# Optimization experiments

Measured on AMD Instinct MI355X. Metric: run time of the kernel, lower is better.

The kernel has to match this reference:

```python
import jax, jax.numpy as jnp
import numpy as np

N = 400000
NUM_OBJECTS = 80000
LOSS_WEIGHT = 1.0
EPS_W = 1e-5
EPS_A = 1e-7

X_SIGN = jnp.array([1, 1, -1, -1, 1, 1, -1, -1], dtype=jnp.float32)
Y_SIGN = jnp.array([1, -1, -1, 1, 1, -1, -1, 1], dtype=jnp.float32)
Z_SIGN = jnp.array([1, 1, 1, 1, -1, -1, -1, -1], dtype=jnp.float32)


def setup_inputs() -> dict:
    key = jax.random.key(0)
    k1, k2, k3, k4, k5, k6 = jax.random.split(key, 6)
    # 3D boxes: centers spread in front of the camera, positive sizes, yaw in [-pi, pi]
    xyz = jnp.concatenate([
        jax.random.uniform(k1, (N, 2), minval=-20.0, maxval=20.0),  # x, y lateral
        jax.random.uniform(k2, (N, 1), minval=-1.5, maxval=1.5),    # z
    ], axis=1)
    lwh = jax.random.uniform(k3, (N, 3), minval=1.0, maxval=5.0)
    yaw = jax.random.uniform(k4, (N, 1), minval=-np.pi, maxval=np.pi)
    pred_3d_bboxes = jnp.concatenate([xyz, lwh, yaw], axis=1)  # (N, 7)
    # GT 2D boxes [x1, y1, x2, y2] inside a 1600x900 image
    x1y1 = jax.random.uniform(k5, (N, 2)) * jnp.array([1200.0, 600.0])
    wh2d = jax.random.uniform(jax.random.fold_in(k5, 1), (N, 2), minval=20.0, maxval=300.0)
    gt_2d_bboxes = jnp.concatenate([x1y1, x1y1 + wh2d], axis=1)
    # Projection matrices: pinhole intrinsics * axis swap (lidar x-forward -> cam z), + tiny noise
    fx, fy, cx, cy = 1000.0, 1000.0, 800.0, 450.0
    K = jnp.array([[fx, 0.0, cx, 0.0], [0.0, fy, cy, 0.0], [0.0, 0.0, 1.0, 0.0], [0.0, 0.0, 0.0, 1.0]], dtype=jnp.float32)
    swap = jnp.array([[0.0, -1.0, 0.0, 0.0], [0.0, 0.0, -1.0, 0.0], [1.0, 0.0, 0.0, 60.0], [0.0, 0.0, 0.0, 1.0]], dtype=jnp.float32)
    base = K @ swap  # (4, 4)
    lidar2img = base[None] + 0.01 * jax.random.normal(k6, (N, 4, 4), dtype=jnp.float32)
    img_shapes = jnp.ones((N, 2), dtype=jnp.float32) * jnp.array([900.0, 1600.0], dtype=jnp.float32)
    object_ids = jax.random.randint(jax.random.fold_in(key, 7), (N,), 0, NUM_OBJECTS, dtype=jnp.int32)
    return {
        "pred_3d_bboxes": pred_3d_bboxes,
        "gt_2d_bboxes": gt_2d_bboxes,
        "lidar2img": lidar2img,
        "img_shapes": img_shapes,
        "object_ids": object_ids,
    }


def _corners_from_bboxes_3d(b):
    # b: (N, 7) -> (N, 8, 3)
    x, y, z = b[:, 0], b[:, 1], b[:, 2]
    l, w, h = b[:, 3], b[:, 4], b[:, 5]
    yaw = b[:, 6]
    xc = (l[:, None] / 2) * X_SIGN  # (N, 8)
    yc = (w[:, None] / 2) * Y_SIGN
    zc = (h[:, None] / 2) * Z_SIGN
    corners = jnp.stack([xc, yc, zc], axis=1)  # (N, 3, 8)
    c, s = jnp.cos(yaw), jnp.sin(yaw)
    zero, one = jnp.zeros_like(c), jnp.ones_like(c)
    R = jnp.stack([c, -s, zero, s, c, zero, zero, zero, one], axis=1).reshape(-1, 3, 3)
    corners = jnp.einsum('nij,njk->nik', R, corners)  # (N, 3, 8)
    center = jnp.stack([x, y, z], axis=1)[:, :, None]
    return (corners + center).transpose(0, 2, 1)  # (N, 8, 3)


def _giou(pred, gt):
    x1 = jnp.maximum(pred[:, 0], gt[:, 0])
    y1 = jnp.maximum(pred[:, 1], gt[:, 1])
    x2 = jnp.minimum(pred[:, 2], gt[:, 2])
    y2 = jnp.minimum(pred[:, 3], gt[:, 3])
    inter = jnp.maximum(x2 - x1, 0.0) * jnp.maximum(y2 - y1, 0.0)
    pa = (pred[:, 2] - pred[:, 0]) * (pred[:, 3] - pred[:, 1])
    ga = (gt[:, 2] - gt[:, 0]) * (gt[:, 3] - gt[:, 1])
    union = pa + ga - inter + EPS_A
    iou = inter / union
    cx1 = jnp.minimum(pred[:, 0], gt[:, 0])
    cy1 = jnp.minimum(pred[:, 1], gt[:, 1])
    cx2 = jnp.maximum(pred[:, 2], gt[:, 2])
    cy2 = jnp.maximum(pred[:, 3], gt[:, 3])
    c_area = jnp.maximum(cx2 - cx1, 0.0) * jnp.maximum(cy2 - cy1, 0.0) + EPS_A
    return iou - (c_area - union) / c_area


def _loss(pred_3d_bboxes, gt_2d_bboxes, lidar2img, img_shapes, object_ids):
    corners = _corners_from_bboxes_3d(pred_3d_bboxes)  # (N, 8, 3)
    ones = jnp.ones(corners.shape[:2] + (1,), dtype=corners.dtype)
    hom = jnp.concatenate([corners, ones], axis=2)  # (N, 8, 4)
    img_hom = jnp.einsum('nij,nkj->nki', lidar2img, hom)  # (N, 8, 4)
    w = jnp.maximum(img_hom[..., 2], EPS_W)  # (N, 8)
    x_img = img_hom[..., 0] / w
    y_img = img_hom[..., 1] / w
    H, W = img_shapes[:, 0], img_shapes[:, 1]
    min_x = jnp.clip(jnp.min(x_img, axis=1), 0.0, W)
    max_x = jnp.clip(jnp.max(x_img, axis=1), 0.0, W)
    min_y = jnp.clip(jnp.min(y_img, axis=1), 0.0, H)
    max_y = jnp.clip(jnp.max(y_img, axis=1), 0.0, H)
    pred_2d = jnp.stack([min_x, min_y, max_x, max_y], axis=1)  # (N, 4)
    loss = 1.0 - _giou(pred_2d, gt_2d_bboxes)  # (N,)
    # per-object mean over views, then mean over unique (present) objects
    sums = jax.ops.segment_sum(loss, object_ids, num_segments=NUM_OBJECTS)
    counts = jax.ops.segment_sum(jnp.ones_like(loss), object_ids, num_segments=NUM_OBJECTS)
    seg_mean = sums / jnp.maximum(counts, 1.0)
    present = counts > 0
    per_obj = jnp.sum(jnp.where(present, seg_mean, 0.0)) / jnp.sum(present.astype(loss.dtype))
    return LOSS_WEIGHT * per_obj


def reference(pred_3d_bboxes, gt_2d_bboxes, lidar2img, img_shapes, object_ids):
    return _loss(pred_3d_bboxes, gt_2d_bboxes, lidar2img, img_shapes, object_ids)
```

## Files before the change

### kernel.cpp

```cpp
#include <hip/hip_runtime.h>
#include <hip/hip_bf16.h>
#include <math.h>

#define NUM_OBJECTS 80000
#define EPS_W 1e-5f
#define EPS_A 1e-7f

#define LOSS_SCALE_F 262144.0f
#define INV_LOSS_SCALE_F (1.0f / 262144.0f)

#define ZERO_VEC16 20001

__global__ void zero_ws(uint4* __restrict__ ws) {
    int i = blockIdx.x * blockDim.x + threadIdx.x;
    if (i < ZERO_VEC16) {
        ws[i] = make_uint4(0u, 0u, 0u, 0u);
    }
}

__global__ void __launch_bounds__(256) loss_kernel(
        const float* __restrict__ pred,
        const float* __restrict__ gt2d,
        const float* __restrict__ l2i,
        const float* __restrict__ imgsh,
        const int*   __restrict__ ids,
        unsigned int* __restrict__ table,
        int n) {
    int t = blockIdx.x * blockDim.x + threadIdx.x;
    int i0 = t * 4;
    if (i0 >= n) return;

    float p[28];
    {
        const float4* pp = (const float4*)(pred + (size_t)i0 * 7);
        float4 P0 = pp[0], P1 = pp[1], P2 = pp[2], P3 = pp[3];
        float4 P4 = pp[4], P5 = pp[5], P6 = pp[6];
        p[0]=P0.x; p[1]=P0.y; p[2]=P0.z; p[3]=P0.w;
        p[4]=P1.x; p[5]=P1.y; p[6]=P1.z; p[7]=P1.w;
        p[8]=P2.x; p[9]=P2.y; p[10]=P2.z; p[11]=P2.w;
        p[12]=P3.x; p[13]=P3.y; p[14]=P3.z; p[15]=P3.w;
        p[16]=P4.x; p[17]=P4.y; p[18]=P4.z; p[19]=P4.w;
        p[20]=P5.x; p[21]=P5.y; p[22]=P5.z; p[23]=P5.w;
        p[24]=P6.x; p[25]=P6.y; p[26]=P6.z; p[27]=P6.w;
    }
    int4 id4 = *(const int4*)(ids + i0);
    int idv[4] = {id4.x, id4.y, id4.z, id4.w};

    const float XS[8] = {1.f, 1.f, -1.f, -1.f, 1.f, 1.f, -1.f, -1.f};
    const float YS[8] = {1.f, -1.f, -1.f, 1.f, 1.f, -1.f, -1.f, 1.f};
    const float ZS[8] = {1.f, 1.f, 1.f, 1.f, -1.f, -1.f, -1.f, -1.f};

#pragma unroll
    for (int j = 0; j < 4; ++j) {
        int i = i0 + j;
        if (i >= n) break;
        float x = p[7*j+0], y = p[7*j+1], z = p[7*j+2];
        float hl = 0.5f * p[7*j+3], hw = 0.5f * p[7*j+4], hh = 0.5f * p[7*j+5];
        float yaw = p[7*j+6];
        float s, c;
        __sincosf(yaw, &s, &c);

        const float4* M = (const float4*)(l2i + 16 * (size_t)i);
        float4 M0 = M[0];
        float4 M1 = M[1];
        float4 M2 = M[2];

        float minx = 1e30f, maxx = -1e30f, miny = 1e30f, maxy = -1e30f;
#pragma unroll
        for (int k = 0; k < 8; ++k) {
            float xc = hl * XS[k];
            float yc = hw * YS[k];
            float zc = hh * ZS[k];
            float cx = c * xc - s * yc + x;
            float cy = s * xc + c * yc + y;
            float cz = zc + z;
            float X  = M0.x * cx + M0.y * cy + M0.z * cz + M0.w;
            float Y  = M1.x * cx + M1.y * cy + M1.z * cz + M1.w;
            float Wc = M2.x * cx + M2.y * cy + M2.z * cz + M2.w;
            float wd = fmaxf(Wc, EPS_W);
            float xi = X / wd;
            float yi = Y / wd;
            minx = fminf(minx, xi); maxx = fmaxf(maxx, xi);
            miny = fminf(miny, yi); maxy = fmaxf(maxy, yi);
        }

        float2 hwd = ((const float2*)imgsh)[i];
        float H = hwd.x, W = hwd.y;
        float px1 = fminf(fmaxf(minx, 0.f), W);
        float px2 = fminf(fmaxf(maxx, 0.f), W);
        float py1 = fminf(fmaxf(miny, 0.f), H);
        float py2 = fminf(fmaxf(maxy, 0.f), H);

        float4 g = ((const float4*)gt2d)[i];

        float ix1 = fmaxf(px1, g.x);
        float iy1 = fmaxf(py1, g.y);
        float ix2 = fminf(px2, g.z);
        float iy2 = fminf(py2, g.w);
        float inter = fmaxf(ix2 - ix1, 0.f) * fmaxf(iy2 - iy1, 0.f);
        float pa = (px2 - px1) * (py2 - py1);
        float ga = (g.z - g.x) * (g.w - g.y);
        float uni = pa + ga - inter + EPS_A;
        float iou = inter / uni;

        float cx1 = fminf(px1, g.x);
        float cy1 = fminf(py1, g.y);
        float cx2 = fmaxf(px2, g.z);
        float cy2 = fmaxf(py2, g.w);
        float carea = fmaxf(cx2 - cx1, 0.f) * fmaxf(cy2 - cy1, 0.f) + EPS_A;
        float giou = iou - (carea - uni) / carea;
        float loss = 1.0f - giou;

        unsigned int fixedp = (unsigned int)(loss * LOSS_SCALE_F + 0.5f);
        atomicAdd(&table[idv[j]], (fixedp << 8) | 1u);
    }
}

__global__ void __launch_bounds__(256) seg_reduce(
        const uint4* __restrict__ table4,
        float* __restrict__ acc,
        unsigned int* __restrict__ ticket,
        float* __restrict__ out) {
    int i = blockIdx.x * blockDim.x + threadIdx.x;
    float sm = 0.f, pr = 0.f;
    if (i < NUM_OBJECTS / 4) {
        uint4 pk = table4[i];
        unsigned int w0 = pk.x, w1 = pk.y, w2 = pk.z, w3 = pk.w;
        unsigned int c0 = w0 & 0xFFu, c1 = w1 & 0xFFu, c2 = w2 & 0xFFu, c3 = w3 & 0xFFu;
        if (c0) { sm += (float)(w0 >> 8) * INV_LOSS_SCALE_F / (float)c0; pr += 1.f; }
        if (c1) { sm += (float)(w1 >> 8) * INV_LOSS_SCALE_F / (float)c1; pr += 1.f; }
        if (c2) { sm += (float)(w2 >> 8) * INV_LOSS_SCALE_F / (float)c2; pr += 1.f; }
        if (c3) { sm += (float)(w3 >> 8) * INV_LOSS_SCALE_F / (float)c3; pr += 1.f; }
    }
#pragma unroll
    for (int off = 32; off > 0; off >>= 1) {
        sm += __shfl_down(sm, off);
        pr += __shfl_down(pr, off);
    }
    __shared__ float ssm[4], spr[4];
    int lane = threadIdx.x & 63;
    int wid = threadIdx.x >> 6;
    if (lane == 0) { ssm[wid] = sm; spr[wid] = pr; }
    __syncthreads();
    if (threadIdx.x == 0) {
        float a = 0.f, b2 = 0.f;
#pragma unroll
        for (int k = 0; k < 4; ++k) { a += ssm[k]; b2 += spr[k]; }
        atomicAdd(&acc[0], a);
        atomicAdd(&acc[1], b2);
        __threadfence();
        unsigned int old = atomicAdd(ticket, 1u);
        if (old == gridDim.x - 1) {
            float s = atomicAdd(&acc[0], 0.f);
            float pcnt = atomicAdd(&acc[1], 0.f);
            out[0] = s / pcnt;
        }
    }
}

extern "C" void kernel_launch(void* const* d_in, const int* in_sizes, int n_in,
                              void* d_out, int out_size, void* d_ws, size_t ws_size,
                              hipStream_t stream) {
    const float* pred  = (const float*)d_in[0];
    const float* gt2d  = (const float*)d_in[1];
    const float* l2i   = (const float*)d_in[2];
    const float* imgsh = (const float*)d_in[3];
    const int*   ids   = (const int*)d_in[4];
    float* out = (float*)d_out;

    int n = in_sizes[0] / 7;

    unsigned int* table  = (unsigned int*)d_ws;
    float*        acc    = (float*)(table + NUM_OBJECTS);
    unsigned int* ticket = (unsigned int*)(acc + 2);

    int block = 256;

    int gridz = (ZERO_VEC16 + block - 1) / block;
    zero_ws<<<gridz, block, 0, stream>>>((uint4*)d_ws);

    int nthreads = (n + 3) / 4;
    int grid1 = (nthreads + block - 1) / block;
    loss_kernel<<<grid1, block, 0, stream>>>(pred, gt2d, l2i, imgsh, ids, table, n);

    int grid2 = (NUM_OBJECTS / 4 + block - 1) / block;
    seg_reduce<<<grid2, block, 0, stream>>>((const uint4*)table, acc, ticket, out);
}
```

Before: 36.06 us.

## Privatize segment accumulation table per XCD with workgroup-scope atomics

Each block reads its XCC id from a hardware register and accumulates into a private per-XCD copy of the segment table, using relaxed atomics at workgroup scope so they can stay in the local L2 instead of going device-wide. The reduction kernel then sums the eight copies per object before computing means. This targets the cost of device-coherent atomics crossing XCDs. In exchange it zeros and reads eight times more workspace, and it depends on workgroup-scope atomics on one XCD's L2 being correctly visible to the next kernel and on the XCC id register encoding being right.

```diff
diff --git a/kernel.cpp b/kernel.cpp
--- a/kernel.cpp
+++ b/kernel.cpp
@@ -9,15 +9,16 @@
 #define LOSS_SCALE_F 262144.0f
 #define INV_LOSS_SCALE_F (1.0f / 262144.0f)
 
-#define ZERO_VEC16 20001
-
-__global__ void zero_ws(uint4* __restrict__ ws) {
+#define XCC_ID_GETREG (((4 - 1) << 11) | (0 << 6) | 20)
+
+__global__ void zero_ws(uint4* __restrict__ ws, int nvec) {
     int i = blockIdx.x * blockDim.x + threadIdx.x;
-    if (i < ZERO_VEC16) {
+    if (i < nvec) {
         ws[i] = make_uint4(0u, 0u, 0u, 0u);
     }
 }
 
+template <int NT>
 __global__ void __launch_bounds__(256) loss_kernel(
         const float* __restrict__ pred,
         const float* __restrict__ gt2d,
@@ -29,6 +30,14 @@
     int t = blockIdx.x * blockDim.x + threadIdx.x;
     int i0 = t * 4;
     if (i0 >= n) return;
+
+    unsigned int* tab;
+    if (NT == 8) {
+        unsigned int xcc = __builtin_amdgcn_s_getreg(XCC_ID_GETREG) & 7u;
+        tab = table + (size_t)xcc * NUM_OBJECTS;
+    } else {
+        tab = table;
+    }
 
     float p[28];
     {
@@ -111,26 +120,39 @@
         float giou = iou - (carea - uni) / carea;
         float loss = 1.0f - giou;
 
-        unsigned int fixedp = (unsigned int)(loss * LOSS_SCALE_F + 0.5f);
-        atomicAdd(&table[idv[j]], (fixedp << 8) | 1u);
-    }
-}
-
+        unsigned int pk = ((unsigned int)(loss * LOSS_SCALE_F + 0.5f) << 8) | 1u;
+        if (NT == 8) {
+            __hip_atomic_fetch_add(&tab[idv[j]], pk, __ATOMIC_RELAXED,
+                                   __HIP_MEMORY_SCOPE_WORKGROUP);
+        } else {
+            atomicAdd(&tab[idv[j]], pk);
+        }
+    }
+}
+
+template <int NT>
 __global__ void __launch_bounds__(256) seg_reduce(
-        const uint4* __restrict__ table4,
+        const unsigned int* __restrict__ table,
         float* __restrict__ acc,
         unsigned int* __restrict__ ticket,
         float* __restrict__ out) {
     int i = blockIdx.x * blockDim.x + threadIdx.x;
     float sm = 0.f, pr = 0.f;
     if (i < NUM_OBJECTS / 4) {
-        uint4 pk = table4[i];
-        unsigned int w0 = pk.x, w1 = pk.y, w2 = pk.z, w3 = pk.w;
-        unsigned int c0 = w0 & 0xFFu, c1 = w1 & 0xFFu, c2 = w2 & 0xFFu, c3 = w3 & 0xFFu;
-        if (c0) { sm += (float)(w0 >> 8) * INV_LOSS_SCALE_F / (float)c0; pr += 1.f; }
-        if (c1) { sm += (float)(w1 >> 8) * INV_LOSS_SCALE_F / (float)c1; pr += 1.f; }
-        if (c2) { sm += (float)(w2 >> 8) * INV_LOSS_SCALE_F / (float)c2; pr += 1.f; }
-        if (c3) { sm += (float)(w3 >> 8) * INV_LOSS_SCALE_F / (float)c3; pr += 1.f; }
+        unsigned int sf0 = 0, sf1 = 0, sf2 = 0, sf3 = 0;
+        unsigned int c0 = 0, c1 = 0, c2 = 0, c3 = 0;
+#pragma unroll
+        for (int tt = 0; tt < NT; ++tt) {
+            uint4 pk = ((const uint4*)(table + (size_t)tt * NUM_OBJECTS))[i];
+            sf0 += pk.x >> 8; c0 += pk.x & 0xFFu;
+            sf1 += pk.y >> 8; c1 += pk.y & 0xFFu;
+            sf2 += pk.z >> 8; c2 += pk.z & 0xFFu;
+            sf3 += pk.w >> 8; c3 += pk.w & 0xFFu;
+        }
+        if (c0) { sm += (float)sf0 * INV_LOSS_SCALE_F / (float)c0; pr += 1.f; }
+        if (c1) { sm += (float)sf1 * INV_LOSS_SCALE_F / (float)c1; pr += 1.f; }
+        if (c2) { sm += (float)sf2 * INV_LOSS_SCALE_F / (float)c2; pr += 1.f; }
+        if (c3) { sm += (float)sf3 * INV_LOSS_SCALE_F / (float)c3; pr += 1.f; }
     }
 #pragma unroll
     for (int off = 32; off > 0; off >>= 1) {
@@ -169,20 +191,28 @@
     float* out = (float*)d_out;
 
     int n = in_sizes[0] / 7;
+    int block = 256;
+
+    bool xcd8 = ws_size >= (size_t)8 * NUM_OBJECTS * sizeof(unsigned int) + 16;
+    int nt = xcd8 ? 8 : 1;
 
     unsigned int* table  = (unsigned int*)d_ws;
-    float*        acc    = (float*)(table + NUM_OBJECTS);
+    float*        acc    = (float*)(table + (size_t)nt * NUM_OBJECTS);
     unsigned int* ticket = (unsigned int*)(acc + 2);
 
-    int block = 256;
-
-    int gridz = (ZERO_VEC16 + block - 1) / block;
-    zero_ws<<<gridz, block, 0, stream>>>((uint4*)d_ws);
+    int nvec = (nt * NUM_OBJECTS * 4 + 16) / 16;
+    int gridz = (nvec + block - 1) / block;
+    zero_ws<<<gridz, block, 0, stream>>>((uint4*)d_ws, nvec);
 
     int nthreads = (n + 3) / 4;
     int grid1 = (nthreads + block - 1) / block;
-    loss_kernel<<<grid1, block, 0, stream>>>(pred, gt2d, l2i, imgsh, ids, table, n);
-
     int grid2 = (NUM_OBJECTS / 4 + block - 1) / block;
-    seg_reduce<<<grid2, block, 0, stream>>>((const uint4*)table, acc, ticket, out);
-}
+
+    if (xcd8) {
+        loss_kernel<8><<<grid1, block, 0, stream>>>(pred, gt2d, l2i, imgsh, ids, table, n);
+        seg_reduce<8><<<grid2, block, 0, stream>>>(table, acc, ticket, out);
+    } else {
+        loss_kernel<1><<<grid1, block, 0, stream>>>(pred, gt2d, l2i, imgsh, ids, table, n);
+        seg_reduce<1><<<grid2, block, 0, stream>>>(table, acc, ticket, out);
+    }
+}
```

After: 36.80 us. 2.1% more time.
